# Optimization experiments

Hardware: AMD Instinct MI355X
Metric: run time of the kernel (lower is better)

The kernel has to match this reference:

```python
import jax, jax.numpy as jnp
import numpy as np

N_NODES = 50000
N_EDGES = 2000000
IN_DIM = 64
N_B = 32


def setup_inputs() -> dict:
    key = jax.random.key(0)
    k1, k2, k3, k4 = jax.random.split(key, 4)
    Eu = jax.random.normal(k1, (N_NODES, IN_DIM), dtype=jnp.float32)
    Ev = jax.random.normal(k2, (N_NODES, IN_DIM), dtype=jnp.float32)
    edge_index = jax.random.randint(k3, (2, N_EDGES), 0, N_NODES, dtype=jnp.int64)
    # xavier_uniform_ on [n_b, in_dim]: bound = sqrt(6/(n_b+in_dim))
    bound = float(np.sqrt(6.0 / (N_B + IN_DIM)))
    E_b = jax.random.uniform(k4, (N_B, IN_DIM), dtype=jnp.float32, minval=-bound, maxval=bound)
    return {"Eu": Eu, "Ev": Ev, "edge_index": edge_index, "E_b": E_b}


def reference(Eu, Ev, edge_index, E_b):
    src, dst = edge_index[0], edge_index[1]
    r = Eu[src] * Ev[dst]                      # [E, d] edge gather + hadamard
    logits = jnp.einsum('ed,bd->eb', r, E_b)   # [E, n_b]
    alpha = jax.nn.softmax(logits, axis=-1)    # [E, n_b]
    w = jnp.einsum('eb,bd->ed', alpha, E_b)    # [E, d]
    score = jax.nn.sigmoid(jnp.sum(r * w, axis=-1))  # [E]
    return jnp.clip(score, 0.0, 1.0)
```

## Files before the change

### kernel.cpp

```cpp
#include <hip/hip_runtime.h>

#define NB 32
#define DIM 64

typedef _Float16 half8_t __attribute__((ext_vector_type(8)));
typedef float floatx4 __attribute__((ext_vector_type(4)));

__global__ __launch_bounds__(256) void cvt_f16_kernel(
    const float* __restrict__ Eu, const float* __restrict__ Ev,
    const float* __restrict__ E_b,
    _Float16* __restrict__ EuH, _Float16* __restrict__ EvH,
    _Float16* __restrict__ EbH, int n8)
{
    int i = blockIdx.x * blockDim.x + threadIdx.x;
    if (i < n8) {
        const float4* u4 = (const float4*)Eu + 2 * i;
        const float4* v4 = (const float4*)Ev + 2 * i;
        float4 a0 = u4[0], a1 = u4[1];
        float4 b0 = v4[0], b1 = v4[1];
        half8_t hu, hv;
        hu[0] = (_Float16)a0.x; hu[1] = (_Float16)a0.y; hu[2] = (_Float16)a0.z; hu[3] = (_Float16)a0.w;
        hu[4] = (_Float16)a1.x; hu[5] = (_Float16)a1.y; hu[6] = (_Float16)a1.z; hu[7] = (_Float16)a1.w;
        hv[0] = (_Float16)b0.x; hv[1] = (_Float16)b0.y; hv[2] = (_Float16)b0.z; hv[3] = (_Float16)b0.w;
        hv[4] = (_Float16)b1.x; hv[5] = (_Float16)b1.y; hv[6] = (_Float16)b1.z; hv[7] = (_Float16)b1.w;
        ((half8_t*)EuH)[i] = hu;
        ((half8_t*)EvH)[i] = hv;
    }
    if (blockIdx.x == 0) {
        int base = threadIdx.x * 8;
        if (base < NB * DIM) {
            const float4* b4 = (const float4*)(E_b + base);
            float4 x0 = b4[0], x1 = b4[1];
            half8_t h;
            h[0] = (_Float16)x0.x; h[1] = (_Float16)x0.y; h[2] = (_Float16)x0.z; h[3] = (_Float16)x0.w;
            h[4] = (_Float16)x1.x; h[5] = (_Float16)x1.y; h[6] = (_Float16)x1.z; h[7] = (_Float16)x1.w;
            *(half8_t*)(EbH + base) = h;
        }
    }
}

__global__ __launch_bounds__(256, 4) void ptt_mfma_kernel(
    const _Float16* __restrict__ EuH, const _Float16* __restrict__ EvH,
    const int* __restrict__ edge_index,
    const _Float16* __restrict__ EbH,
    float* __restrict__ out, int E)
{
    const int lane = threadIdx.x & 63;
    const int wave = threadIdx.x >> 6;
    const int j16 = lane & 15;
    const int g = lane >> 4;
    const int eb = (blockIdx.x * 4 + wave) * 64;

    int isrc[4], idst[4];
#pragma unroll
    for (int t = 0; t < 4; ++t) {
        int e = eb + t * 16 + j16;
        int ec = e < E ? e : (E - 1);
        isrc[t] = __builtin_nontemporal_load(edge_index + ec);
        idst[t] = __builtin_nontemporal_load(edge_index + E + ec);
    }

    half8_t Af[2][2];
#pragma unroll
    for (int mt = 0; mt < 2; ++mt)
#pragma unroll
        for (int ks = 0; ks < 2; ++ks)
            Af[mt][ks] = *(const half8_t*)(EbH + (mt * 16 + j16) * DIM + ks * 32 + g * 8);

    const char* ub = (const char*)EuH;
    const char* vb = (const char*)EvH;
    half8_t u[4][2], v[4][2];
#pragma unroll
    for (int t = 0; t < 4; ++t) {
        unsigned su = (unsigned)isrc[t] * (DIM * 2u) + (unsigned)(g * 16);
        unsigned sv = (unsigned)idst[t] * (DIM * 2u) + (unsigned)(g * 16);
#pragma unroll
        for (int ks = 0; ks < 2; ++ks) {
            u[t][ks] = *(const half8_t*)(ub + (su + ks * 64u));
            v[t][ks] = *(const half8_t*)(vb + (sv + ks * 64u));
        }
    }

    floatx4 acc[4][2];
#pragma unroll
    for (int t = 0; t < 4; ++t) {
        acc[t][0] = (floatx4){0.f, 0.f, 0.f, 0.f};
        acc[t][1] = (floatx4){0.f, 0.f, 0.f, 0.f};
    }

#pragma unroll
    for (int t = 0; t < 4; ++t)
#pragma unroll
        for (int ks = 0; ks < 2; ++ks) {
            half8_t r = u[t][ks] * v[t][ks];
            acc[t][0] = __builtin_amdgcn_mfma_f32_16x16x32_f16(Af[0][ks], r, acc[t][0], 0, 0, 0);
            acc[t][1] = __builtin_amdgcn_mfma_f32_16x16x32_f16(Af[1][ks], r, acc[t][1], 0, 0, 0);
        }

#pragma unroll
    for (int t = 0; t < 4; ++t) {
        float s1 = 0.f, s2 = 0.f;
#pragma unroll
        for (int mt = 0; mt < 2; ++mt)
#pragma unroll
            for (int q = 0; q < 4; ++q) {
                float a = acc[t][mt][q];
                float p = __expf(a);
                s1 += p;
                s2 = fmaf(p, a, s2);
            }
        s1 += __shfl_xor(s1, 16);
        s2 += __shfl_xor(s2, 16);
        s1 += __shfl_xor(s1, 32);
        s2 += __shfl_xor(s2, 32);
        float x = __fdividef(s2, s1);
        float score = __fdividef(1.0f, 1.0f + __expf(-x));
        if (lane < 16) {
            int eo = eb + t * 16 + j16;
            if (eo < E) __builtin_nontemporal_store(score, out + eo);
        }
    }
}

__global__ __launch_bounds__(256) void ptt_mfma_f32_kernel(
    const float* __restrict__ Eu, const float* __restrict__ Ev,
    const int* __restrict__ edge_index,
    const float* __restrict__ E_b,
    float* __restrict__ out, int E)
{
    const int lane = threadIdx.x & 63;
    const int wave = threadIdx.x >> 6;
    const int j16 = lane & 15;
    const int g = lane >> 4;
    const int eb = (blockIdx.x * 4 + wave) * 64;

    half8_t Af[2][2];
#pragma unroll
    for (int mt = 0; mt < 2; ++mt)
#pragma unroll
        for (int ks = 0; ks < 2; ++ks) {
            const float* p = E_b + (mt * 16 + j16) * DIM + ks * 32 + g * 8;
            float4 x0 = ((const float4*)p)[0];
            float4 x1 = ((const float4*)p)[1];
            half8_t h;
            h[0] = (_Float16)x0.x; h[1] = (_Float16)x0.y; h[2] = (_Float16)x0.z; h[3] = (_Float16)x0.w;
            h[4] = (_Float16)x1.x; h[5] = (_Float16)x1.y; h[6] = (_Float16)x1.z; h[7] = (_Float16)x1.w;
            Af[mt][ks] = h;
        }

    floatx4 acc[4][2];
#pragma unroll
    for (int t = 0; t < 4; ++t) {
        acc[t][0] = (floatx4){0.f, 0.f, 0.f, 0.f};
        acc[t][1] = (floatx4){0.f, 0.f, 0.f, 0.f};
    }

#pragma unroll
    for (int t = 0; t < 4; ++t) {
        int e = eb + t * 16 + j16;
        int ec = e < E ? e : (E - 1);
        int src = edge_index[ec];
        int dst = edge_index[E + ec];
#pragma unroll
        for (int ks = 0; ks < 2; ++ks) {
            const float4* up = (const float4*)(Eu + (long long)src * DIM + ks * 32 + g * 8);
            const float4* vp = (const float4*)(Ev + (long long)dst * DIM + ks * 32 + g * 8);
            float4 u0 = up[0], u1 = up[1];
            float4 v0 = vp[0], v1 = vp[1];
            half8_t r;
            r[0] = (_Float16)(u0.x * v0.x); r[1] = (_Float16)(u0.y * v0.y);
            r[2] = (_Float16)(u0.z * v0.z); r[3] = (_Float16)(u0.w * v0.w);
            r[4] = (_Float16)(u1.x * v1.x); r[5] = (_Float16)(u1.y * v1.y);
            r[6] = (_Float16)(u1.z * v1.z); r[7] = (_Float16)(u1.w * v1.w);
            acc[t][0] = __builtin_amdgcn_mfma_f32_16x16x32_f16(Af[0][ks], r, acc[t][0], 0, 0, 0);
            acc[t][1] = __builtin_amdgcn_mfma_f32_16x16x32_f16(Af[1][ks], r, acc[t][1], 0, 0, 0);
        }
    }

#pragma unroll
    for (int t = 0; t < 4; ++t) {
        float s1 = 0.f, s2 = 0.f;
#pragma unroll
        for (int mt = 0; mt < 2; ++mt)
#pragma unroll
            for (int q = 0; q < 4; ++q) {
                float a = acc[t][mt][q];
                float p = __expf(a);
                s1 += p;
                s2 = fmaf(p, a, s2);
            }
        s1 += __shfl_xor(s1, 16);
        s2 += __shfl_xor(s2, 16);
        s1 += __shfl_xor(s1, 32);
        s2 += __shfl_xor(s2, 32);
        float x = __fdividef(s2, s1);
        float score = __fdividef(1.0f, 1.0f + __expf(-x));
        if (lane < 16) {
            int eo = eb + t * 16 + j16;
            if (eo < E) out[eo] = score;
        }
    }
}

extern "C" void kernel_launch(void* const* d_in, const int* in_sizes, int n_in,
                              void* d_out, int out_size, void* d_ws, size_t ws_size,
                              hipStream_t stream) {
    const float* Eu = (const float*)d_in[0];
    const float* Ev = (const float*)d_in[1];
    const int* edge_index = (const int*)d_in[2];
    const float* E_b = (const float*)d_in[3];
    float* out = (float*)d_out;

    int n_nodes_elems = in_sizes[0];
    int n_edges = in_sizes[2] / 2;
    size_t need = (size_t)(2 * n_nodes_elems + NB * DIM) * sizeof(_Float16);

    int block = 256;
    int grid = (n_edges + 255) / 256;

    if (ws_size >= need) {
        _Float16* EuH = (_Float16*)d_ws;
        _Float16* EvH = EuH + n_nodes_elems;
        _Float16* EbH = EvH + n_nodes_elems;
        int n8 = n_nodes_elems / 8;
        cvt_f16_kernel<<<(n8 + 255) / 256, 256, 0, stream>>>(Eu, Ev, E_b, EuH, EvH, EbH, n8);
        ptt_mfma_kernel<<<grid, block, 0, stream>>>(EuH, EvH, edge_index, EbH, out, n_edges);
    } else {
        ptt_mfma_f32_kernel<<<grid, block, 0, stream>>>(Eu, Ev, edge_index, E_b, out, n_edges);
    }
}
```

Before: 87.56 us.

## Bucket-sort edges by source node before gather to improve locality

Measured after the change: 171.8 us. 96.2% more time.

```diff
diff --git a/kernel.cpp b/kernel.cpp
--- a/kernel.cpp
+++ b/kernel.cpp
@@ -2,9 +2,13 @@
 
 #define NB 32
 #define DIM 64
+#define BSHIFT 6
+#define MAXBUCK 1024
+#define SEPB 8
 
 typedef _Float16 half8_t __attribute__((ext_vector_type(8)));
 typedef float floatx4 __attribute__((ext_vector_type(4)));
+typedef int int2v __attribute__((ext_vector_type(2)));
 
 __global__ __launch_bounds__(256) void cvt_f16_kernel(
     const float* __restrict__ Eu, const float* __restrict__ Ev,
@@ -35,6 +39,172 @@
             h[0] = (_Float16)x0.x; h[1] = (_Float16)x0.y; h[2] = (_Float16)x0.z; h[3] = (_Float16)x0.w;
             h[4] = (_Float16)x1.x; h[5] = (_Float16)x1.y; h[6] = (_Float16)x1.z; h[7] = (_Float16)x1.w;
             *(half8_t*)(EbH + base) = h;
+        }
+    }
+}
+
+__global__ __launch_bounds__(256) void hist_kernel(
+    const int* __restrict__ edge_index, int E, int nbuck,
+    unsigned* __restrict__ ghist)
+{
+    __shared__ unsigned h[MAXBUCK];
+    for (int i = threadIdx.x; i < nbuck; i += blockDim.x) h[i] = 0u;
+    __syncthreads();
+    for (int e = blockIdx.x * blockDim.x + threadIdx.x; e < E;
+         e += gridDim.x * blockDim.x) {
+        int s = __builtin_nontemporal_load(edge_index + e);
+        atomicAdd(&h[s >> BSHIFT], 1u);
+    }
+    __syncthreads();
+    for (int i = threadIdx.x; i < nbuck; i += blockDim.x)
+        if (h[i]) atomicAdd(&ghist[i], h[i]);
+}
+
+__global__ __launch_bounds__(1024) void scan_kernel(
+    const unsigned* __restrict__ ghist, int nbuck,
+    unsigned* __restrict__ cursor)
+{
+    __shared__ unsigned a[MAXBUCK], b[MAXBUCK];
+    int t = threadIdx.x;
+    unsigned own = (t < nbuck) ? ghist[t] : 0u;
+    a[t] = own;
+    __syncthreads();
+    unsigned* pin = a; unsigned* pout = b;
+    for (int off = 1; off < MAXBUCK; off <<= 1) {
+        unsigned x = pin[t] + ((t >= off) ? pin[t - off] : 0u);
+        pout[t] = x;
+        __syncthreads();
+        unsigned* tmp = pin; pin = pout; pout = tmp;
+    }
+    if (t < nbuck) cursor[t] = pin[t] - own;
+}
+
+__global__ __launch_bounds__(512) void scatter_kernel(
+    const int* __restrict__ edge_index, int E, int nbuck,
+    unsigned* __restrict__ cursor,
+    int2v* __restrict__ sSD, int* __restrict__ sId)
+{
+    __shared__ unsigned lcnt[MAXBUCK];
+    __shared__ unsigned lbase[MAXBUCK];
+    for (int i = threadIdx.x; i < nbuck; i += 512) lcnt[i] = 0u;
+    __syncthreads();
+
+    int e0 = blockIdx.x * (512 * SEPB);
+    int src_[SEPB], dst_[SEPB];
+#pragma unroll
+    for (int k = 0; k < SEPB; ++k) {
+        int e = e0 + k * 512 + threadIdx.x;
+        if (e < E) {
+            src_[k] = __builtin_nontemporal_load(edge_index + e);
+            dst_[k] = __builtin_nontemporal_load(edge_index + E + e);
+            atomicAdd(&lcnt[src_[k] >> BSHIFT], 1u);
+        }
+    }
+    __syncthreads();
+    for (int i = threadIdx.x; i < nbuck; i += 512) {
+        unsigned c = lcnt[i];
+        lbase[i] = c ? atomicAdd(&cursor[i], c) : 0u;
+    }
+    __syncthreads();
+    for (int i = threadIdx.x; i < nbuck; i += 512) lcnt[i] = 0u;
+    __syncthreads();
+#pragma unroll
+    for (int k = 0; k < SEPB; ++k) {
+        int e = e0 + k * 512 + threadIdx.x;
+        if (e < E) {
+            int bk = src_[k] >> BSHIFT;
+            unsigned r = atomicAdd(&lcnt[bk], 1u);
+            unsigned pos = lbase[bk] + r;
+            int2v p; p.x = src_[k]; p.y = dst_[k];
+            sSD[pos] = p;
+            sId[pos] = e;
+        }
+    }
+}
+
+__global__ __launch_bounds__(256, 4) void ptt_mfma_sorted_kernel(
+    const _Float16* __restrict__ EuH, const _Float16* __restrict__ EvH,
+    const int2v* __restrict__ sSD, const int* __restrict__ sId,
+    const _Float16* __restrict__ EbH,
+    float* __restrict__ out, int E)
+{
+    const int lane = threadIdx.x & 63;
+    const int wave = threadIdx.x >> 6;
+    const int j16 = lane & 15;
+    const int g = lane >> 4;
+    const int eb = (blockIdx.x * 4 + wave) * 64;
+
+    int2v sd[4]; int iid[4];
+#pragma unroll
+    for (int t = 0; t < 4; ++t) {
+        int e = eb + t * 16 + j16;
+        int ec = e < E ? e : (E - 1);
+        sd[t] = __builtin_nontemporal_load(sSD + ec);
+        iid[t] = __builtin_nontemporal_load(sId + ec);
+    }
+
+    half8_t Af[2][2];
+#pragma unroll
+    for (int mt = 0; mt < 2; ++mt)
+#pragma unroll
+        for (int ks = 0; ks < 2; ++ks)
+            Af[mt][ks] = *(const half8_t*)(EbH + (mt * 16 + j16) * DIM + ks * 32 + g * 8);
+
+    const char* ub = (const char*)EuH;
+    const char* vb = (const char*)EvH;
+    half8_t u[4][2], v[4][2];
+#pragma unroll
+    for (int t = 0; t < 4; ++t) {
+        unsigned sv = (unsigned)sd[t].y * (DIM * 2u) + (unsigned)(g * 16);
+#pragma unroll
+        for (int ks = 0; ks < 2; ++ks)
+            v[t][ks] = *(const half8_t*)(vb + (sv + ks * 64u));
+    }
+#pragma unroll
+    for (int t = 0; t < 4; ++t) {
+        unsigned su = (unsigned)sd[t].x * (DIM * 2u) + (unsigned)(g * 16);
+#pragma unroll
+        for (int ks = 0; ks < 2; ++ks)
+            u[t][ks] = *(const half8_t*)(ub + (su + ks * 64u));
+    }
+
+    floatx4 acc[4][2];
+#pragma unroll
+    for (int t = 0; t < 4; ++t) {
+        acc[t][0] = (floatx4){0.f, 0.f, 0.f, 0.f};
+        acc[t][1] = (floatx4){0.f, 0.f, 0.f, 0.f};
+    }
+
+#pragma unroll
+    for (int t = 0; t < 4; ++t)
+#pragma unroll
+        for (int ks = 0; ks < 2; ++ks) {
+            half8_t r = u[t][ks] * v[t][ks];
+            acc[t][0] = __builtin_amdgcn_mfma_f32_16x16x32_f16(Af[0][ks], r, acc[t][0], 0, 0, 0);
+            acc[t][1] = __builtin_amdgcn_mfma_f32_16x16x32_f16(Af[1][ks], r, acc[t][1], 0, 0, 0);
+        }
+
+#pragma unroll
+    for (int t = 0; t < 4; ++t) {
+        float s1 = 0.f, s2 = 0.f;
+#pragma unroll
+        for (int mt = 0; mt < 2; ++mt)
+#pragma unroll
+            for (int q = 0; q < 4; ++q) {
+                float a = acc[t][mt][q];
+                float p = __expf(a);
+                s1 += p;
+                s2 = fmaf(p, a, s2);
+            }
+        s1 += __shfl_xor(s1, 16);
+        s2 += __shfl_xor(s2, 16);
+        s1 += __shfl_xor(s1, 32);
+        s2 += __shfl_xor(s2, 32);
+        float x = __fdividef(s2, s1);
+        float score = __fdividef(1.0f, 1.0f + __expf(-x));
+        if (lane < 16) {
+            int eo = eb + t * 16 + j16;
+            if (eo < E) __builtin_nontemporal_store(score, out + iid[t]);
         }
     }
 }
@@ -122,85 +292,7 @@
     }
 }
 
-__global__ __launch_bounds__(256) void ptt_mfma_f32_kernel(
-    const float* __restrict__ Eu, const float* __restrict__ Ev,
-    const int* __restrict__ edge_index,
-    const float* __restrict__ E_b,
-    float* __restrict__ out, int E)
-{
-    const int lane = threadIdx.x & 63;
-    const int wave = threadIdx.x >> 6;
-    const int j16 = lane & 15;
-    const int g = lane >> 4;
-    const int eb = (blockIdx.x * 4 + wave) * 64;
-
-    half8_t Af[2][2];
-#pragma unroll
-    for (int mt = 0; mt < 2; ++mt)
-#pragma unroll
-        for (int ks = 0; ks < 2; ++ks) {
-            const float* p = E_b + (mt * 16 + j16) * DIM + ks * 32 + g * 8;
-            float4 x0 = ((const float4*)p)[0];
-            float4 x1 = ((const float4*)p)[1];
-            half8_t h;
-            h[0] = (_Float16)x0.x; h[1] = (_Float16)x0.y; h[2] = (_Float16)x0.z; h[3] = (_Float16)x0.w;
-            h[4] = (_Float16)x1.x; h[5] = (_Float16)x1.y; h[6] = (_Float16)x1.z; h[7] = (_Float16)x1.w;
-            Af[mt][ks] = h;
-        }
-
-    floatx4 acc[4][2];
-#pragma unroll
-    for (int t = 0; t < 4; ++t) {
-        acc[t][0] = (floatx4){0.f, 0.f, 0.f, 0.f};
-        acc[t][1] = (floatx4){0.f, 0.f, 0.f, 0.f};
-    }
-
-#pragma unroll
-    for (int t = 0; t < 4; ++t) {
-        int e = eb + t * 16 + j16;
-        int ec = e < E ? e : (E - 1);
-        int src = edge_index[ec];
-        int dst = edge_index[E + ec];
-#pragma unroll
-        for (int ks = 0; ks < 2; ++ks) {
-            const float4* up = (const float4*)(Eu + (long long)src * DIM + ks * 32 + g * 8);
-            const float4* vp = (const float4*)(Ev + (long long)dst * DIM + ks * 32 + g * 8);
-            float4 u0 = up[0], u1 = up[1];
-            float4 v0 = vp[0], v1 = vp[1];
-            half8_t r;
-            r[0] = (_Float16)(u0.x * v0.x); r[1] = (_Float16)(u0.y * v0.y);
-            r[2] = (_Float16)(u0.z * v0.z); r[3] = (_Float16)(u0.w * v0.w);
-            r[4] = (_Float16)(u1.x * v1.x); r[5] = (_Float16)(u1.y * v1.y);
-            r[6] = (_Float16)(u1.z * v1.z); r[7] = (_Float16)(u1.w * v1.w);
-            acc[t][0] = __builtin_amdgcn_mfma_f32_16x16x32_f16(Af[0][ks], r, acc[t][0], 0, 0, 0);
-            acc[t][1] = __builtin_amdgcn_mfma_f32_16x16x32_f16(Af[1][ks], r, acc[t][1], 0, 0, 0);
-        }
-    }
-
-#pragma unroll
-    for (int t = 0; t < 4; ++t) {
-        float s1 = 0.f, s2 = 0.f;
-#pragma unroll
-        for (int mt = 0; mt < 2; ++mt)
-#pragma unroll
-            for (int q = 0; q < 4; ++q) {
-                float a = acc[t][mt][q];
-                float p = __expf(a);
-                s1 += p;
-                s2 = fmaf(p, a, s2);
-            }
-        s1 += __shfl_xor(s1, 16);
-        s2 += __shfl_xor(s2, 16);
-        s1 += __shfl_xor(s1, 32);
-        s2 += __shfl_xor(s2, 32);
-        float x = __fdividef(s2, s1);
-        float score = __fdividef(1.0f, 1.0f + __expf(-x));
-        if (lane < 16) {
-            int eo = eb + t * 16 + j16;
-            if (eo < E) out[eo] = score;
-        }
-    }
-}
+static inline size_t align256(size_t x) { return (x + 255) & ~(size_t)255; }
 
 extern "C" void kernel_launch(void* const* d_in, const int* in_sizes, int n_in,
                               void* d_out, int out_size, void* d_ws, size_t ws_size,
@@ -212,20 +304,47 @@
     float* out = (float*)d_out;
 
     int n_nodes_elems = in_sizes[0];
-    int n_edges = in_sizes[2] / 2;
-    size_t need = (size_t)(2 * n_nodes_elems + NB * DIM) * sizeof(_Float16);
-
-    int block = 256;
-    int grid = (n_edges + 255) / 256;
-
-    if (ws_size >= need) {
-        _Float16* EuH = (_Float16*)d_ws;
+    int n_nodes = n_nodes_elems / DIM;
+    int E = in_sizes[2] / 2;
+    int nbuck = (n_nodes + (1 << BSHIFT) - 1) >> BSHIFT;
+
+    size_t off = 0;
+    size_t o_EuH = off; off = align256(off + (size_t)n_nodes_elems * 2);
+    size_t o_EvH = off; off = align256(off + (size_t)n_nodes_elems * 2);
+    size_t o_EbH = off; off = align256(off + (size_t)NB * DIM * 2);
+    size_t o_hist = off; off = align256(off + (size_t)MAXBUCK * 4);
+    size_t o_cur  = off; off = align256(off + (size_t)MAXBUCK * 4);
+    size_t o_sSD  = off; off = align256(off + (size_t)E * 8);
+    size_t o_sId  = off; off = align256(off + (size_t)E * 4);
+    size_t need_full = off;
+    size_t need_fp16 = align256((size_t)n_nodes_elems * 2) * 2 + 4096;
+
+    char* w = (char*)d_ws;
+    int grid = (E + 255) / 256;
+
+    if (ws_size >= need_full && nbuck <= MAXBUCK) {
+        _Float16* EuH = (_Float16*)(w + o_EuH);
+        _Float16* EvH = (_Float16*)(w + o_EvH);
+        _Float16* EbH = (_Float16*)(w + o_EbH);
+        unsigned* hist = (unsigned*)(w + o_hist);
+        unsigned* cursor = (unsigned*)(w + o_cur);
+        int2v* sSD = (int2v*)(w + o_sSD);
+        int* sId = (int*)(w + o_sId);
+
+        int n8 = n_nodes_elems / 8;
+        cvt_f16_kernel<<<(n8 + 255) / 256, 256, 0, stream>>>(Eu, Ev, E_b, EuH, EvH, EbH, n8);
+        (void)hipMemsetAsync(hist, 0, (size_t)MAXBUCK * 4, stream);
+        hist_kernel<<<512, 256, 0, stream>>>(edge_index, E, nbuck, hist);
+        scan_kernel<<<1, 1024, 0, stream>>>(hist, nbuck, cursor);
+        int sblocks = (E + 512 * SEPB - 1) / (512 * SEPB);
+        scatter_kernel<<<sblocks, 512, 0, stream>>>(edge_index, E, nbuck, cursor, sSD, sId);
+        ptt_mfma_sorted_kernel<<<grid, 256, 0, stream>>>(EuH, EvH, sSD, sId, EbH, out, E);
+    } else if (ws_size >= need_fp16) {
+        _Float16* EuH = (_Float16*)w;
         _Float16* EvH = EuH + n_nodes_elems;
         _Float16* EbH = EvH + n_nodes_elems;
         int n8 = n_nodes_elems / 8;
         cvt_f16_kernel<<<(n8 + 255) / 256, 256, 0, stream>>>(Eu, Ev, E_b, EuH, EvH, EbH, n8);
-        ptt_mfma_kernel<<<grid, block, 0, stream>>>(EuH, EvH, edge_index, EbH, out, n_edges);
-    } else {
-        ptt_mfma_f32_kernel<<<grid, block, 0, stream>>>(Eu, Ev, edge_index, E_b, out, n_edges);
-    }
-}
+        ptt_mfma_kernel<<<grid, 256, 0, stream>>>(EuH, EvH, edge_index, EbH, out, E);
+    }
+}
```

## Partition edges by destination node range per XCD for L2 locality

Applied to the files above, without the earlier changes.

Measured after the change: 111.1 us. 26.9% more time.

```diff
diff --git a/kernel.cpp b/kernel.cpp
--- a/kernel.cpp
+++ b/kernel.cpp
@@ -2,6 +2,8 @@
 
 #define NB 32
 #define DIM 64
+#define TILE 2048
+#define NXCD 8
 
 typedef _Float16 half8_t __attribute__((ext_vector_type(8)));
 typedef float floatx4 __attribute__((ext_vector_type(4)));
@@ -39,6 +41,145 @@
     }
 }
 
+__global__ __launch_bounds__(256, 4) void ptt_filter_kernel(
+    const _Float16* __restrict__ EuH, const _Float16* __restrict__ EvH,
+    const int* __restrict__ edge_index, const _Float16* __restrict__ EbH,
+    float* __restrict__ out, int E, int n_nodes)
+{
+    __shared__ int qs[TILE], qd[TILE], qi[TILE];
+    __shared__ int wsum[4];
+
+    const int tid = threadIdx.x;
+    const int lane = tid & 63;
+    const int wave = tid >> 6;
+    const int g = blockIdx.x & (NXCD - 1);
+    const int e0 = (blockIdx.x >> 3) * TILE;
+
+    const int lo = (int)((long long)g * n_nodes / NXCD);
+    const int hi = (int)((long long)(g + 1) * n_nodes / NXCD);
+
+    int src8[8], dst8[8];
+    bool mk[8];
+    int m8 = 0;
+#pragma unroll
+    for (int k = 0; k < 8; ++k) {
+        int e = e0 + k * 256 + tid;
+        int ec = e < E ? e : (E - 1);
+        src8[k] = __builtin_nontemporal_load(edge_index + ec);
+        dst8[k] = __builtin_nontemporal_load(edge_index + E + ec);
+        mk[k] = (e < E) & (dst8[k] >= lo) & (dst8[k] < hi);
+        m8 += mk[k] ? 1 : 0;
+    }
+    int pre = m8;
+#pragma unroll
+    for (int d = 1; d < 64; d <<= 1) {
+        int n = __shfl_up(pre, d);
+        if (lane >= d) pre += n;
+    }
+    if (lane == 63) wsum[wave] = pre;
+    __syncthreads();
+    int wbase = 0;
+#pragma unroll
+    for (int w = 0; w < 4; ++w) wbase += (w < wave) ? wsum[w] : 0;
+    const int qc = wsum[0] + wsum[1] + wsum[2] + wsum[3];
+    int off = wbase + pre - m8;
+#pragma unroll
+    for (int k = 0; k < 8; ++k) {
+        if (mk[k]) {
+            qs[off] = src8[k];
+            qd[off] = dst8[k];
+            qi[off] = e0 + k * 256 + tid;
+            ++off;
+        }
+    }
+    __syncthreads();
+    if (qc == 0) return;
+
+    const int j16 = lane & 15;
+    const int gg = lane >> 4;
+
+    half8_t Af[2][2];
+#pragma unroll
+    for (int mt = 0; mt < 2; ++mt)
+#pragma unroll
+        for (int ks = 0; ks < 2; ++ks)
+            Af[mt][ks] = *(const half8_t*)(EbH + (mt * 16 + j16) * DIM + ks * 32 + gg * 8);
+
+    int per = (qc + 3) >> 2;
+    per = (per + 15) & ~15;
+    const int q0 = wave * per;
+    const int q1 = (q0 + per < qc) ? (q0 + per) : qc;
+    if (q0 >= qc) return;
+
+    const char* ub = (const char*)EuH;
+    const char* vb = (const char*)EvH;
+
+    for (int base = q0; base < q1; base += 64) {
+        int ss[4], dd[4], ii[4];
+#pragma unroll
+        for (int t = 0; t < 4; ++t) {
+            int qx = base + t * 16 + j16;
+            int qxc = qx < q1 ? qx : (q1 - 1);
+            ss[t] = qs[qxc];
+            dd[t] = qd[qxc];
+            ii[t] = qi[qxc];
+        }
+
+        half8_t u[4][2], v[4][2];
+#pragma unroll
+        for (int t = 0; t < 4; ++t) {
+            unsigned sv = (unsigned)dd[t] * (DIM * 2u) + (unsigned)(gg * 16);
+#pragma unroll
+            for (int ks = 0; ks < 2; ++ks)
+                v[t][ks] = *(const half8_t*)(vb + (sv + ks * 64u));
+        }
+#pragma unroll
+        for (int t = 0; t < 4; ++t) {
+            unsigned su = (unsigned)ss[t] * (DIM * 2u) + (unsigned)(gg * 16);
+#pragma unroll
+            for (int ks = 0; ks < 2; ++ks)
+                u[t][ks] = *(const half8_t*)(ub + (su + ks * 64u));
+        }
+
+        floatx4 acc[4][2];
+#pragma unroll
+        for (int t = 0; t < 4; ++t) {
+            acc[t][0] = (floatx4){0.f, 0.f, 0.f, 0.f};
+            acc[t][1] = (floatx4){0.f, 0.f, 0.f, 0.f};
+        }
+#pragma unroll
+        for (int t = 0; t < 4; ++t)
+#pragma unroll
+            for (int ks = 0; ks < 2; ++ks) {
+                half8_t r = u[t][ks] * v[t][ks];
+                acc[t][0] = __builtin_amdgcn_mfma_f32_16x16x32_f16(Af[0][ks], r, acc[t][0], 0, 0, 0);
+                acc[t][1] = __builtin_amdgcn_mfma_f32_16x16x32_f16(Af[1][ks], r, acc[t][1], 0, 0, 0);
+            }
+
+#pragma unroll
+        for (int t = 0; t < 4; ++t) {
+            float s1 = 0.f, s2 = 0.f;
+#pragma unroll
+            for (int mt = 0; mt < 2; ++mt)
+#pragma unroll
+                for (int q = 0; q < 4; ++q) {
+                    float a = acc[t][mt][q];
+                    float p = __expf(a);
+                    s1 += p;
+                    s2 = fmaf(p, a, s2);
+                }
+            s1 += __shfl_xor(s1, 16);
+            s2 += __shfl_xor(s2, 16);
+            s1 += __shfl_xor(s1, 32);
+            s2 += __shfl_xor(s2, 32);
+            float x = __fdividef(s2, s1);
+            float score = __fdividef(1.0f, 1.0f + __expf(-x));
+            if (lane < 16 && (base + t * 16 + j16) < q1)
+                __builtin_nontemporal_store(score, out + ii[t]);
+        }
+    }
+}
+
 __global__ __launch_bounds__(256, 4) void ptt_mfma_kernel(
     const _Float16* __restrict__ EuH, const _Float16* __restrict__ EvH,
     const int* __restrict__ edge_index,
@@ -87,7 +228,6 @@
         acc[t][0] = (floatx4){0.f, 0.f, 0.f, 0.f};
         acc[t][1] = (floatx4){0.f, 0.f, 0.f, 0.f};
     }
-
 #pragma unroll
     for (int t = 0; t < 4; ++t)
 #pragma unroll
@@ -122,85 +262,7 @@
     }
 }
 
-__global__ __launch_bounds__(256) void ptt_mfma_f32_kernel(
-    const float* __restrict__ Eu, const float* __restrict__ Ev,
-    const int* __restrict__ edge_index,
-    const float* __restrict__ E_b,
-    float* __restrict__ out, int E)
-{
-    const int lane = threadIdx.x & 63;
-    const int wave = threadIdx.x >> 6;
-    const int j16 = lane & 15;
-    const int g = lane >> 4;
-    const int eb = (blockIdx.x * 4 + wave) * 64;
-
-    half8_t Af[2][2];
-#pragma unroll
-    for (int mt = 0; mt < 2; ++mt)
-#pragma unroll
-        for (int ks = 0; ks < 2; ++ks) {
-            const float* p = E_b + (mt * 16 + j16) * DIM + ks * 32 + g * 8;
-            float4 x0 = ((const float4*)p)[0];
-            float4 x1 = ((const float4*)p)[1];
-            half8_t h;
-            h[0] = (_Float16)x0.x; h[1] = (_Float16)x0.y; h[2] = (_Float16)x0.z; h[3] = (_Float16)x0.w;
-            h[4] = (_Float16)x1.x; h[5] = (_Float16)x1.y; h[6] = (_Float16)x1.z; h[7] = (_Float16)x1.w;
-            Af[mt][ks] = h;
-        }
-
-    floatx4 acc[4][2];
-#pragma unroll
-    for (int t = 0; t < 4; ++t) {
-        acc[t][0] = (floatx4){0.f, 0.f, 0.f, 0.f};
-        acc[t][1] = (floatx4){0.f, 0.f, 0.f, 0.f};
-    }
-
-#pragma unroll
-    for (int t = 0; t < 4; ++t) {
-        int e = eb + t * 16 + j16;
-        int ec = e < E ? e : (E - 1);
-        int src = edge_index[ec];
-        int dst = edge_index[E + ec];
-#pragma unroll
-        for (int ks = 0; ks < 2; ++ks) {
-            const float4* up = (const float4*)(Eu + (long long)src * DIM + ks * 32 + g * 8);
-            const float4* vp = (const float4*)(Ev + (long long)dst * DIM + ks * 32 + g * 8);
-            float4 u0 = up[0], u1 = up[1];
-            float4 v0 = vp[0], v1 = vp[1];
-            half8_t r;
-            r[0] = (_Float16)(u0.x * v0.x); r[1] = (_Float16)(u0.y * v0.y);
-            r[2] = (_Float16)(u0.z * v0.z); r[3] = (_Float16)(u0.w * v0.w);
-            r[4] = (_Float16)(u1.x * v1.x); r[5] = (_Float16)(u1.y * v1.y);
-            r[6] = (_Float16)(u1.z * v1.z); r[7] = (_Float16)(u1.w * v1.w);
-            acc[t][0] = __builtin_amdgcn_mfma_f32_16x16x32_f16(Af[0][ks], r, acc[t][0], 0, 0, 0);
-            acc[t][1] = __builtin_amdgcn_mfma_f32_16x16x32_f16(Af[1][ks], r, acc[t][1], 0, 0, 0);
-        }
-    }
-
-#pragma unroll
-    for (int t = 0; t < 4; ++t) {
-        float s1 = 0.f, s2 = 0.f;
-#pragma unroll
-        for (int mt = 0; mt < 2; ++mt)
-#pragma unroll
-            for (int q = 0; q < 4; ++q) {
-                float a = acc[t][mt][q];
-                float p = __expf(a);
-                s1 += p;
-                s2 = fmaf(p, a, s2);
-            }
-        s1 += __shfl_xor(s1, 16);
-        s2 += __shfl_xor(s2, 16);
-        s1 += __shfl_xor(s1, 32);
-        s2 += __shfl_xor(s2, 32);
-        float x = __fdividef(s2, s1);
-        float score = __fdividef(1.0f, 1.0f + __expf(-x));
-        if (lane < 16) {
-            int eo = eb + t * 16 + j16;
-            if (eo < E) out[eo] = score;
-        }
-    }
-}
+static inline size_t align256(size_t x) { return (x + 255) & ~(size_t)255; }
 
 extern "C" void kernel_launch(void* const* d_in, const int* in_sizes, int n_in,
                               void* d_out, int out_size, void* d_ws, size_t ws_size,
@@ -212,20 +274,22 @@
     float* out = (float*)d_out;
 
     int n_nodes_elems = in_sizes[0];
-    int n_edges = in_sizes[2] / 2;
-    size_t need = (size_t)(2 * n_nodes_elems + NB * DIM) * sizeof(_Float16);
-
-    int block = 256;
-    int grid = (n_edges + 255) / 256;
-
-    if (ws_size >= need) {
-        _Float16* EuH = (_Float16*)d_ws;
-        _Float16* EvH = EuH + n_nodes_elems;
-        _Float16* EbH = EvH + n_nodes_elems;
-        int n8 = n_nodes_elems / 8;
-        cvt_f16_kernel<<<(n8 + 255) / 256, 256, 0, stream>>>(Eu, Ev, E_b, EuH, EvH, EbH, n8);
-        ptt_mfma_kernel<<<grid, block, 0, stream>>>(EuH, EvH, edge_index, EbH, out, n_edges);
-    } else {
-        ptt_mfma_f32_kernel<<<grid, block, 0, stream>>>(Eu, Ev, edge_index, E_b, out, n_edges);
-    }
-}
+    int n_nodes = n_nodes_elems / DIM;
+    int E = in_sizes[2] / 2;
+    size_t need = align256((size_t)n_nodes_elems * 2) * 2 +
+                  align256((size_t)NB * DIM * 2);
+
+    if (ws_size < need) return;
+
+    char* w = (char*)d_ws;
+    _Float16* EuH = (_Float16*)w;
+    _Float16* EvH = (_Float16*)(w + align256((size_t)n_nodes_elems * 2));
+    _Float16* EbH = (_Float16*)(w + align256((size_t)n_nodes_elems * 2) * 2);
+
+    int n8 = n_nodes_elems / 8;
+    cvt_f16_kernel<<<(n8 + 255) / 256, 256, 0, stream>>>(Eu, Ev, E_b, EuH, EvH, EbH, n8);
+
+    int ntiles = (E + TILE - 1) / TILE;
+    int grid = ntiles * NXCD;
+    ptt_filter_kernel<<<grid, 256, 0, stream>>>(EuH, EvH, edge_index, EbH, out, E, n_nodes);
+}
```
